# Kernel optimization log

Measured on AMD Instinct MI355X. Metric: run time of the kernel, lower is better.

The kernel has to match this reference:

```python
import jax, jax.numpy as jnp
import numpy as np

DIM = 2048
NUM_HEADS = 16
NUM_KV_HEADS = 4
HEAD_DIM = DIM // NUM_HEADS  # 128
ROPE_BASE = 10000.0
TRAIN_SEQ_LEN = 1024
EPS = 1.1920929e-07  # torch.finfo(float32).eps, used by F.rms_norm default


def _rope_tables(seq_len, dtype=jnp.float32):
    rd = HEAD_DIM  # rope_dims defaults to full head_dim
    if seq_len > TRAIN_SEQ_LEN:
        s = seq_len / TRAIN_SEQ_LEN
        base = ROPE_BASE * s ** (rd / (rd - 2))
    else:
        base = ROPE_BASE
    inv_freq = 1.0 / base ** (jnp.arange(0, rd, 2, dtype=jnp.float32) / rd)
    t = jnp.arange(seq_len, dtype=jnp.float32)
    freqs = jnp.outer(t, inv_freq)  # [S, rd//2]
    cos = jnp.cos(freqs)[None, :, None, :].astype(dtype)  # [1,S,1,rd//2]
    sin = jnp.sin(freqs)[None, :, None, :].astype(dtype)
    return cos, sin


def _rms_norm(x):
    var = jnp.mean(jnp.square(x), axis=-1, keepdims=True)
    return x * jax.lax.rsqrt(var + EPS)


def _apply_rotary(x, cos, sin):
    h = x.shape[-1] // 2
    x1, x2 = x[..., :h], x[..., h:]
    return jnp.concatenate((x1 * cos + x2 * sin, -x1 * sin + x2 * cos), axis=-1)


def setup_inputs() -> dict:
    key = jax.random.key(0)
    ks = jax.random.split(key, 6)
    B, S = 2, 2048
    kv_dim = NUM_KV_HEADS * HEAD_DIM
    x = jax.random.normal(ks[0], (B, S, DIM), dtype=jnp.float32)
    Wq = jax.random.normal(ks[1], (DIM, DIM), dtype=jnp.float32) * 0.02
    Wk = jax.random.normal(ks[2], (kv_dim, DIM), dtype=jnp.float32) * 0.02
    Wv = jax.random.normal(ks[3], (kv_dim, DIM), dtype=jnp.float32) * 0.02
    Wo = jax.random.normal(ks[4], (DIM, DIM), dtype=jnp.float32) * 0.02
    q_gain = jnp.full((NUM_HEADS,), 1.0, dtype=jnp.float32)
    return {"x": x, "Wq": Wq, "Wk": Wk, "Wv": Wv, "Wo": Wo, "q_gain": q_gain}


def reference(x, Wq, Wk, Wv, Wo, q_gain):
    B, S, D = x.shape
    H, Hkv, Dh = NUM_HEADS, NUM_KV_HEADS, HEAD_DIM
    # QKV projections (CastedLinear, no bias)
    q = (x @ Wq.T).reshape(B, S, H, Dh)
    k = (x @ Wk.T).reshape(B, S, Hkv, Dh)
    v = (x @ Wv.T).reshape(B, S, Hkv, Dh)
    # RMSNorm over head_dim (no learned weight)
    q = _rms_norm(q)
    k = _rms_norm(k)
    # RoPE (full head_dim, NTK-scaled since S > train_seq_len)
    cos, sin = _rope_tables(S, q.dtype)
    q = _apply_rotary(q, cos, sin)
    k = _apply_rotary(k, cos, sin)
    # per-head gain on q
    q = q * q_gain.astype(q.dtype)[None, None, :, None]
    # GQA: repeat_interleave kv heads
    reps = H // Hkv
    k = jnp.repeat(k, reps, axis=2)  # [B,S,H,Dh]
    v = jnp.repeat(v, reps, axis=2)
    # causal attention
    scale = 1.0 / jnp.sqrt(jnp.asarray(Dh, dtype=q.dtype))
    scores = jnp.einsum('bqhd,bkhd->bhqk', q, k) * scale  # [B,H,S,S]
    causal = jnp.tril(jnp.ones((S, S), dtype=bool))
    scores = jnp.where(causal[None, None], scores, jnp.finfo(scores.dtype).min)
    attn = jax.nn.softmax(scores, axis=-1)
    y = jnp.einsum('bhqk,bkhd->bqhd', attn, v)  # [B,S,H,Dh]
    return y.reshape(B, S, D) @ Wo.T
```

## Files before the change

### kernel.cpp

```cpp
#include <hip/hip_runtime.h>

#define DIMSZ 2048
#define NHEAD 16
#define NKV 4
#define HD 128
#define QKVD 3072
#define SEQ 2048
#define NTOK 4096

typedef __attribute__((ext_vector_type(8))) short short8;
typedef __attribute__((ext_vector_type(4))) float f32x4;
typedef unsigned short u16;

__device__ __forceinline__ u16 f2bf(float x) {
  union { float f; unsigned u; } v; v.f = x;
  unsigned r = v.u + 0x7fffu + ((v.u >> 16) & 1u);
  return (u16)(r >> 16);
}
__device__ __forceinline__ unsigned pack_bf2(float a, float b) {
  unsigned ua = __float_as_uint(a) + 0x8000u;
  unsigned ub = __float_as_uint(b) + 0x8000u;
  return __builtin_amdgcn_perm(ub, ua, 0x07060302);
}

__device__ __forceinline__ void gl_lds16(const void* g, void* l) {
  __builtin_amdgcn_global_load_lds(
      (const __attribute__((address_space(1))) void*)g,
      (__attribute__((address_space(3))) void*)l, 16, 0, 0);
}

__global__ __launch_bounds__(256)
void castAll(const float* __restrict__ x,  const float* __restrict__ Wq,
             const float* __restrict__ Wk, const float* __restrict__ Wv,
             const float* __restrict__ Wo, u16* __restrict__ xb,
             u16* __restrict__ Wqkvb, u16* __restrict__ Wob) {
  int i = blockIdx.x * 256 + threadIdx.x;
  int f = i * 4;
  const float* src; u16* dst; int off;
  if (f < 8388608)       { src = x;  dst = xb;    off = f; }
  else if (f < 12582912) { src = Wq; dst = Wqkvb; off = f - 8388608; }
  else if (f < 13631488) { src = Wk; dst = Wqkvb + 4194304; off = f - 12582912; }
  else if (f < 14680064) { src = Wv; dst = Wqkvb + 5242880; off = f - 13631488; }
  else                   { src = Wo; dst = Wob;   off = f - 14680064; }
  float4 v = *(const float4*)(src + off);
  ushort4 o;
  o.x = f2bf(v.x); o.y = f2bf(v.y); o.z = f2bf(v.z); o.w = f2bf(v.w);
  *(ushort4*)(dst + off) = o;
}

template <bool F32OUT>
__global__ __launch_bounds__(512, 2)
void gemm256(const u16* __restrict__ A, const u16* __restrict__ W,
             void* __restrict__ Cv, int M, int N, int K) {
  __shared__ __align__(16) u16 As[2][256][64];
  __shared__ __align__(16) u16 Bs[2][256][64];
  const int tid = threadIdx.x;
  const int l = tid & 63;
  const int w = tid >> 6;
  const int r = l & 15, q = l >> 4;
  const int wm = (w >> 2) * 128;
  const int wn = (w & 3) * 64;

  const int nx  = N >> 8;
  const int cpx = gridDim.x >> 3;
  const int lid = (blockIdx.x & 7) * cpx + (blockIdx.x >> 3);
  const int m0 = (lid / nx) << 8;
  const int n0 = (lid % nx) << 8;

  const int srow = w * 16 + (l >> 3);
  const int scol = ((l & 7) ^ (l >> 3)) << 3;
  const u16* Asrc = A + (long)(m0 + srow) * K + scol;
  const u16* Bsrc = W + (long)(n0 + srow) * K + scol;

  auto stA = [&](int d, int h, int kt) {
    const u16* s = Asrc + (long)(h * 128) * K + (long)kt * 64;
    gl_lds16(s,         &As[d][h * 128 + w * 16][0]);
    gl_lds16(s + 8 * K, &As[d][h * 128 + w * 16 + 8][0]);
  };
  auto stB = [&](int d, int h, int kt) {
    const u16* s = Bsrc + (long)(h * 128) * K + (long)kt * 64;
    gl_lds16(s,         &Bs[d][h * 128 + w * 16][0]);
    gl_lds16(s + 8 * K, &Bs[d][h * 128 + w * 16 + 8][0]);
  };
  auto lda = [&](int d, int rt, int ks) -> short8 {
    return *(const short8*)&As[d][wm + rt * 16 + r][(((ks << 2) | q) ^ (r & 7)) << 3];
  };
  auto ldb = [&](int d, int ct, int ks) -> short8 {
    return *(const short8*)&Bs[d][wn + ct * 16 + r][(((ks << 2) | q) ^ (r & 7)) << 3];
  };

  f32x4 acc[8][4] = {};
  short8 a[4][2], b[4][2];

#define MMA8(IB, JB)                                                          \
  do {                                                                        \
    __builtin_amdgcn_s_setprio(1);                                            \
    _Pragma("unroll") for (int i_ = 0; i_ < 4; ++i_)                          \
    _Pragma("unroll") for (int j_ = 0; j_ < 2; ++j_)                          \
    _Pragma("unroll") for (int k_ = 0; k_ < 2; ++k_)                          \
      acc[(IB) + i_][(JB) + j_] = __builtin_amdgcn_mfma_f32_16x16x32_bf16(    \
          a[i_][k_], b[(JB) + j_][k_], acc[(IB) + i_][(JB) + j_], 0, 0, 0);   \
    __builtin_amdgcn_s_setprio(0);                                            \
  } while (0)

#define LGKM0()                                           \
  do {                                                    \
    asm volatile("s_waitcnt lgkmcnt(0)" ::: "memory");    \
    __builtin_amdgcn_sched_barrier(0);                    \
  } while (0)

  stB(0, 0, 0); stA(0, 0, 0); stB(0, 1, 0); stA(0, 1, 0);
  stB(1, 0, 1); stA(1, 0, 1);
  asm volatile("s_waitcnt vmcnt(4)" ::: "memory");
  __builtin_amdgcn_s_barrier();

  const int niter = K >> 7;
  for (int it = 0; it < niter; ++it) {
    const int kt1 = 2 * it + 1, kt2 = 2 * it + 2, kt3 = 2 * it + 3;
    const bool more = (it + 1 < niter);

#pragma unroll
    for (int i = 0; i < 4; ++i) { a[i][0] = lda(0, i, 0); a[i][1] = lda(0, i, 1); }
#pragma unroll
    for (int j = 0; j < 2; ++j) { b[j][0] = ldb(0, j, 0); b[j][1] = ldb(0, j, 1); }
    stB(1, 1, kt1);
    __builtin_amdgcn_s_barrier();
    LGKM0();
    MMA8(0, 0);
    __builtin_amdgcn_s_barrier();

#pragma unroll
    for (int j = 2; j < 4; ++j) { b[j][0] = ldb(0, j, 0); b[j][1] = ldb(0, j, 1); }
    stA(1, 1, kt1);
    __builtin_amdgcn_s_barrier();
    LGKM0();
    MMA8(0, 2);
    __builtin_amdgcn_s_barrier();

#pragma unroll
    for (int i = 0; i < 4; ++i) { a[i][0] = lda(0, i + 4, 0); a[i][1] = lda(0, i + 4, 1); }
    if (more) stB(0, 0, kt2);
    __builtin_amdgcn_s_barrier();
    LGKM0();
    MMA8(4, 2);
    __builtin_amdgcn_s_barrier();

    if (more) stA(0, 0, kt2);
    __builtin_amdgcn_s_barrier();
    MMA8(4, 0);
    if (more) asm volatile("s_waitcnt vmcnt(4)" ::: "memory");
    else      asm volatile("s_waitcnt vmcnt(0)" ::: "memory");
    __builtin_amdgcn_s_barrier();

#pragma unroll
    for (int i = 0; i < 4; ++i) { a[i][0] = lda(1, i, 0); a[i][1] = lda(1, i, 1); }
#pragma unroll
    for (int j = 0; j < 2; ++j) { b[j][0] = ldb(1, j, 0); b[j][1] = ldb(1, j, 1); }
    if (more) stB(0, 1, kt2);
    __builtin_amdgcn_s_barrier();
    LGKM0();
    MMA8(0, 0);
    __builtin_amdgcn_s_barrier();

#pragma unroll
    for (int j = 2; j < 4; ++j) { b[j][0] = ldb(1, j, 0); b[j][1] = ldb(1, j, 1); }
    if (more) stA(0, 1, kt2);
    __builtin_amdgcn_s_barrier();
    LGKM0();
    MMA8(0, 2);
    __builtin_amdgcn_s_barrier();

#pragma unroll
    for (int i = 0; i < 4; ++i) { a[i][0] = lda(1, i + 4, 0); a[i][1] = lda(1, i + 4, 1); }
    if (more) stB(1, 0, kt3);
    __builtin_amdgcn_s_barrier();
    LGKM0();
    MMA8(4, 2);
    __builtin_amdgcn_s_barrier();

    if (more) stA(1, 0, kt3);
    __builtin_amdgcn_s_barrier();
    MMA8(4, 0);
    if (more) asm volatile("s_waitcnt vmcnt(4)" ::: "memory");
    __builtin_amdgcn_s_barrier();
  }
#undef MMA8
#undef LGKM0

#pragma unroll
  for (int i = 0; i < 8; ++i)
#pragma unroll
    for (int j = 0; j < 4; ++j) {
      int row = m0 + wm + i * 16 + q * 4;
      int col = n0 + wn + j * 16 + r;
#pragma unroll
      for (int t = 0; t < 4; ++t) {
        if (F32OUT)
          ((float*)Cv)[(long)(row + t) * N + col] = acc[i][j][t];
        else
          ((u16*)Cv)[(long)(row + t) * N + col] = f2bf(acc[i][j][t]);
      }
    }
}

__global__ __launch_bounds__(256)
void prep(u16* __restrict__ qkv, const float* __restrict__ gain, float qsc,
          u16* __restrict__ vt) {
  if (blockIdx.x < 20480) {
    int gid  = blockIdx.x * 4 + (threadIdx.x >> 6);
    int lane = threadIdx.x & 63;
    int token = gid / 20;
    int idx   = gid % 20;
    int s     = token & (SEQ - 1);
    bool isq  = idx < 16;
    int off   = isq ? idx * HD : 2048 + (idx - 16) * HD;
    float psc = isq ? qsc * gain[idx & 15] : 1.0f;
    u16* p = qkv + (long)token * QKVD + off;
    union { unsigned u; float f; } c1, c2;
    c1.u = ((unsigned)p[lane]) << 16;
    c2.u = ((unsigned)p[lane + 64]) << 16;
    float x1 = c1.f, x2 = c2.f;
    float ss = x1 * x1 + x2 * x2;
#pragma unroll
    for (int d = 1; d < 64; d <<= 1) ss += __shfl_xor(ss, d);
    float rn = rsqrtf(ss * (1.0f / 128.0f) + 1.1920929e-07f) * psc;
    float lb = log2f(10000.0f) + 128.0f / 126.0f;
    float inv_freq = exp2f(-(float)lane * (lb * (1.0f / 64.0f)));
    float ang = (float)s * inv_freq;
    float sn, cs;
    sincosf(ang, &sn, &cs);
    p[lane]      = f2bf((x1 * cs + x2 * sn) * rn);
    p[lane + 64] = f2bf((-x1 * sn + x2 * cs) * rn);
  } else {
    __shared__ u16 T[128 * 72];
    int bid = blockIdx.x - 20480;
    const int k0 = (bid & 31) * 64, hkv = (bid >> 5) & 3, b = bid >> 7;
    const u16* vb = qkv + 2560;
    const int t = threadIdx.x;
    const int key = t & 63, dh0 = (t >> 6) * 32;
#pragma unroll
    for (int c = 0; c < 4; c++) {
      uint4 vv = *(const uint4*)&vb[(long)(b * SEQ + k0 + key) * QKVD + hkv * HD + dh0 + c * 8];
      u16 tmp[8];
      *(uint4*)tmp = vv;
#pragma unroll
      for (int e = 0; e < 8; e++) T[(dh0 + c * 8 + e) * 72 + key] = tmp[e];
    }
    __syncthreads();
    const int dh = t >> 1, half = t & 1;
#pragma unroll
    for (int c = 0; c < 4; c++) {
      uint4 ov = *(const uint4*)&T[dh * 72 + half * 32 + c * 8];
      *(uint4*)&vt[((long)(b * NKV + hkv) * HD + dh) * SEQ + k0 + half * 32 + c * 8] = ov;
    }
  }
}

__global__ __launch_bounds__(256, 4)
void fattn(const u16* __restrict__ qb, const u16* __restrict__ kb,
           const u16* __restrict__ vtg, u16* __restrict__ yb) {
  __shared__ u16 Ks[64 * 128];
  __shared__ u16 Vt[128 * 64];
  __shared__ u16 Ps[64 * 64];
  const int tid  = threadIdx.x;
  const int lane = tid & 63;
  const int w    = tid >> 6;
  const int r = lane & 15, q = lane >> 4;
  const int qt = 31 - (blockIdx.x >> 5);
  const int hb = blockIdx.x & 31;
  const int h  = hb >> 1;
  const int b  = hb & 1;
  const int q0 = qt * 64;
  const int hkv = h >> 2;

  long koff[4], voff[4];
  u16 *kdst[4], *vdst[4];
#pragma unroll
  for (int c = 0; c < 4; c++) {
    int gr = w * 16 + c * 4 + (lane >> 4);
    int s  = lane & 15;
    int kj = (s & 8) | ((s ^ gr) & 7);
    koff[c] = (long)gr * QKVD + hkv * HD + kj * 8;
    kdst[c] = Ks + (w * 16 + c * 4) * 128;
    int dh = (w * 4 + c) * 8 + (lane >> 3);
    int vs = lane & 7;
    int vj = (vs ^ dh) & 7;
    voff[c] = (long)dh * SEQ + vj * 8;
    vdst[c] = Vt + (w * 4 + c) * 8 * 64;
  }
  const u16* vbase = vtg + (long)(b * NKV + hkv) * HD * SEQ;

  short8 qf[4];
#pragma unroll
  for (int ks = 0; ks < 4; ks++)
    qf[ks] = *(const short8*)&qb[(long)(b * SEQ + q0 + w * 16 + r) * QKVD +
                                 h * HD + ks * 32 + q * 8];

  f32x4 oacc[8] = {};
  float l_i = 0.f;
  const int maskbase = q * 4 - w * 16 - r;
  const int psx = (r & 7) << 1;

  for (int k0 = 0; k0 <= q0; k0 += 64) {
    __syncthreads();
    const u16* kb_t = kb + (long)(b * SEQ + k0) * QKVD;
    const u16* vb_t = vbase + k0;
#pragma unroll
    for (int c = 0; c < 4; c++) {
      gl_lds16(kb_t + koff[c], kdst[c]);
      gl_lds16(vb_t + voff[c], vdst[c]);
    }
    __syncthreads();

    const bool maskit = (k0 == q0);

    f32x4 st[4] = {};
#pragma unroll
    for (int jt = 0; jt < 4; jt++)
#pragma unroll
      for (int ks = 0; ks < 4; ks++) {
        int row = jt * 16 + r;
        int j = ks * 4 + q;
        int p = (j & 8) | ((j ^ row) & 7);
        short8 kf = *(const short8*)&Ks[row * 128 + p * 8];
        st[jt] = __builtin_amdgcn_mfma_f32_16x16x32_bf16(kf, qf[ks], st[jt], 0, 0, 0);
      }

    if (maskit) {
#pragma unroll
      for (int jt = 0; jt < 4; jt++)
#pragma unroll
        for (int t = 0; t < 4; t++)
          if (jt * 16 + maskbase + t > 0) st[jt][t] = -3e38f;
    }

#pragma unroll
    for (int jt = 0; jt < 4; jt++) {
#pragma unroll
      for (int t = 0; t < 4; t++) {
        float p = exp2f(st[jt][t]);
        st[jt][t] = p;
      }
      l_i += (st[jt][0] + st[jt][1]) + (st[jt][2] + st[jt][3]);
      uint2 pk;
      pk.x = pack_bf2(st[jt][0], st[jt][1]);
      pk.y = pack_bf2(st[jt][2], st[jt][3]);
      *(uint2*)&Ps[(w * 16 + r) * 64 + ((jt * 4 + q) ^ psx) * 4] = pk;
    }
    asm volatile("s_waitcnt lgkmcnt(0)" ::: "memory");

#pragma unroll
    for (int ks = 0; ks < 2; ks++) {
      short8 pf = *(const short8*)&Ps[(w * 16 + r) * 64 + ((ks * 8 + q * 2) ^ psx) * 4];
#pragma unroll
      for (int n = 0; n < 8; n++) {
        int row = n * 16 + r;
        int j = ks * 4 + q;
        int p = (j ^ row) & 7;
        short8 vf = *(const short8*)&Vt[row * 64 + p * 8];
        oacc[n] = __builtin_amdgcn_mfma_f32_16x16x32_bf16(pf, vf, oacc[n], 0, 0, 0);
      }
    }
  }

  l_i += __shfl_xor(l_i, 16);
  l_i += __shfl_xor(l_i, 32);
  float lb4[4];
#pragma unroll
  for (int t = 0; t < 4; t++) lb4[t] = 1.0f / __shfl(l_i, q * 4 + t);
#pragma unroll
  for (int n = 0; n < 8; n++)
#pragma unroll
    for (int t = 0; t < 4; t++) {
      int row = q0 + w * 16 + q * 4 + t;
      int col = n * 16 + r;
      yb[(long)(b * SEQ + row) * DIMSZ + h * HD + col] = f2bf(oacc[n][t] * lb4[t]);
    }
}

extern "C" void kernel_launch(void* const* d_in, const int* in_sizes, int n_in,
                              void* d_out, int out_size, void* d_ws, size_t ws_size,
                              hipStream_t stream) {
  const float* x  = (const float*)d_in[0];
  const float* Wq = (const float*)d_in[1];
  const float* Wk = (const float*)d_in[2];
  const float* Wv = (const float*)d_in[3];
  const float* Wo = (const float*)d_in[4];
  const float* qg = (const float*)d_in[5];
  float* out = (float*)d_out;

  const long MB = 1024 * 1024;
  char* ws = (char*)d_ws;
  u16* xb    = (u16*)(ws + 0 * MB);
  u16* ybuf  = (u16*)(ws + 0 * MB);
  u16* Wqkvb = (u16*)(ws + 16 * MB);
  u16* Wob   = (u16*)(ws + 28 * MB);
  u16* qkv   = (u16*)(ws + 36 * MB);
  u16* vtg   = (u16*)(ws + 60 * MB);

  castAll<<<18432, 256, 0, stream>>>(x, Wq, Wk, Wv, Wo, xb, Wqkvb, Wob);

  gemm256<false><<<(QKVD / 256) * (NTOK / 256), 512, 0, stream>>>(
      xb, Wqkvb, qkv, NTOK, QKVD, DIMSZ);

  const float qsc = 0.08838834764831845f * 1.44269504088896f;
  prep<<<20736, 256, 0, stream>>>(qkv, qg, qsc, vtg);

  fattn<<<1024, 256, 0, stream>>>(qkv, qkv + 2048, vtg, ybuf);

  gemm256<true><<<(DIMSZ / 256) * (NTOK / 256), 512, 0, stream>>>(
      ybuf, Wob, out, NTOK, DIMSZ, DIMSZ);
}
```

Measured before the change: 329.8 us.

## Interleave LDS fragment loads into MFMA phases of the GEMM main loop

```diff
diff --git a/kernel.cpp b/kernel.cpp
--- a/kernel.cpp
+++ b/kernel.cpp
@@ -90,18 +90,44 @@
   };
 
   f32x4 acc[8][4] = {};
-  short8 a[4][2], b[4][2];
-
-#define MMA8(IB, JB)                                                          \
+  short8 a[4][2];
+  short8 bA[2][2];
+  short8 bB[2][2];
+
+#define MF(va, vb, c) __builtin_amdgcn_mfma_f32_16x16x32_bf16(va, vb, c, 0, 0, 0)
+
+#define PHASE_MMA(IB, JB, BP, INJ)                                            \
   do {                                                                        \
     __builtin_amdgcn_s_setprio(1);                                            \
-    _Pragma("unroll") for (int i_ = 0; i_ < 4; ++i_)                          \
-    _Pragma("unroll") for (int j_ = 0; j_ < 2; ++j_)                          \
-    _Pragma("unroll") for (int k_ = 0; k_ < 2; ++k_)                          \
-      acc[(IB) + i_][(JB) + j_] = __builtin_amdgcn_mfma_f32_16x16x32_bf16(    \
-          a[i_][k_], b[(JB) + j_][k_], acc[(IB) + i_][(JB) + j_], 0, 0, 0);   \
+    _Pragma("unroll") for (int i_ = 0; i_ < 4; ++i_) {                        \
+      acc[(IB)+i_][(JB)+0] = MF(a[i_][0], BP[0][0], acc[(IB)+i_][(JB)+0]);    \
+      acc[(IB)+i_][(JB)+1] = MF(a[i_][0], BP[1][0], acc[(IB)+i_][(JB)+1]);    \
+      acc[(IB)+i_][(JB)+0] = MF(a[i_][1], BP[0][1], acc[(IB)+i_][(JB)+0]);    \
+      acc[(IB)+i_][(JB)+1] = MF(a[i_][1], BP[1][1], acc[(IB)+i_][(JB)+1]);    \
+      INJ(i_)                                                                 \
+    }                                                                         \
     __builtin_amdgcn_s_setprio(0);                                            \
   } while (0)
+
+#define INJ_NONE(i_)
+#define INJ_B23_D0(i_)                                                        \
+  if ((i_) == 0) { bB[0][0] = ldb(0,2,0); bB[0][1] = ldb(0,2,1);              \
+                   bB[1][0] = ldb(0,3,0); bB[1][1] = ldb(0,3,1); }
+#define INJ_A47_D0(i_)                                                        \
+  { a[i_][0] = lda(0,4+(i_),0); a[i_][1] = lda(0,4+(i_),1); }
+#define INJ_P4(i_)                                                            \
+  { a[i_][0] = lda(1,(i_),0); a[i_][1] = lda(1,(i_),1);                       \
+    if ((i_) == 0) { bB[0][0] = ldb(1,0,0); bB[0][1] = ldb(1,0,1);            \
+                     bB[1][0] = ldb(1,1,0); bB[1][1] = ldb(1,1,1); } }
+#define INJ_B23_D1(i_)                                                        \
+  if ((i_) == 0) { bA[0][0] = ldb(1,2,0); bA[0][1] = ldb(1,2,1);              \
+                   bA[1][0] = ldb(1,3,0); bA[1][1] = ldb(1,3,1); }
+#define INJ_A47_D1(i_)                                                        \
+  { a[i_][0] = lda(1,4+(i_),0); a[i_][1] = lda(1,4+(i_),1); }
+#define INJ_P8(i_)                                                            \
+  if (more) { a[i_][0] = lda(0,(i_),0); a[i_][1] = lda(0,(i_),1);             \
+    if ((i_) == 0) { bA[0][0] = ldb(0,0,0); bA[0][1] = ldb(0,0,1);            \
+                     bA[1][0] = ldb(0,1,0); bA[1][1] = ldb(0,1,1); } }
 
 #define LGKM0()                                           \
   do {                                                    \
@@ -113,78 +139,76 @@
   stB(1, 0, 1); stA(1, 0, 1);
   asm volatile("s_waitcnt vmcnt(4)" ::: "memory");
   __builtin_amdgcn_s_barrier();
+#pragma unroll
+  for (int i = 0; i < 4; ++i) { a[i][0] = lda(0, i, 0); a[i][1] = lda(0, i, 1); }
+#pragma unroll
+  for (int j = 0; j < 2; ++j) { bA[j][0] = ldb(0, j, 0); bA[j][1] = ldb(0, j, 1); }
 
   const int niter = K >> 7;
   for (int it = 0; it < niter; ++it) {
     const int kt1 = 2 * it + 1, kt2 = 2 * it + 2, kt3 = 2 * it + 3;
     const bool more = (it + 1 < niter);
 
-#pragma unroll
-    for (int i = 0; i < 4; ++i) { a[i][0] = lda(0, i, 0); a[i][1] = lda(0, i, 1); }
-#pragma unroll
-    for (int j = 0; j < 2; ++j) { b[j][0] = ldb(0, j, 0); b[j][1] = ldb(0, j, 1); }
     stB(1, 1, kt1);
     __builtin_amdgcn_s_barrier();
     LGKM0();
-    MMA8(0, 0);
-    __builtin_amdgcn_s_barrier();
-
-#pragma unroll
-    for (int j = 2; j < 4; ++j) { b[j][0] = ldb(0, j, 0); b[j][1] = ldb(0, j, 1); }
+    PHASE_MMA(0, 0, bA, INJ_B23_D0);
+    __builtin_amdgcn_s_barrier();
+
     stA(1, 1, kt1);
     __builtin_amdgcn_s_barrier();
     LGKM0();
-    MMA8(0, 2);
-    __builtin_amdgcn_s_barrier();
-
-#pragma unroll
-    for (int i = 0; i < 4; ++i) { a[i][0] = lda(0, i + 4, 0); a[i][1] = lda(0, i + 4, 1); }
+    PHASE_MMA(0, 2, bB, INJ_A47_D0);
+    __builtin_amdgcn_s_barrier();
+
     if (more) stB(0, 0, kt2);
     __builtin_amdgcn_s_barrier();
     LGKM0();
-    MMA8(4, 2);
+    PHASE_MMA(4, 2, bB, INJ_NONE);
+    if (more) asm volatile("s_waitcnt vmcnt(2)" ::: "memory");
+    else      asm volatile("s_waitcnt vmcnt(0)" ::: "memory");
     __builtin_amdgcn_s_barrier();
 
     if (more) stA(0, 0, kt2);
     __builtin_amdgcn_s_barrier();
-    MMA8(4, 0);
-    if (more) asm volatile("s_waitcnt vmcnt(4)" ::: "memory");
-    else      asm volatile("s_waitcnt vmcnt(0)" ::: "memory");
-    __builtin_amdgcn_s_barrier();
-
-#pragma unroll
-    for (int i = 0; i < 4; ++i) { a[i][0] = lda(1, i, 0); a[i][1] = lda(1, i, 1); }
-#pragma unroll
-    for (int j = 0; j < 2; ++j) { b[j][0] = ldb(1, j, 0); b[j][1] = ldb(1, j, 1); }
+    LGKM0();
+    PHASE_MMA(4, 0, bA, INJ_P4);
+    __builtin_amdgcn_s_barrier();
+
     if (more) stB(0, 1, kt2);
     __builtin_amdgcn_s_barrier();
     LGKM0();
-    MMA8(0, 0);
-    __builtin_amdgcn_s_barrier();
-
-#pragma unroll
-    for (int j = 2; j < 4; ++j) { b[j][0] = ldb(1, j, 0); b[j][1] = ldb(1, j, 1); }
+    PHASE_MMA(0, 0, bB, INJ_B23_D1);
+    __builtin_amdgcn_s_barrier();
+
     if (more) stA(0, 1, kt2);
     __builtin_amdgcn_s_barrier();
     LGKM0();
-    MMA8(0, 2);
-    __builtin_amdgcn_s_barrier();
-
-#pragma unroll
-    for (int i = 0; i < 4; ++i) { a[i][0] = lda(1, i + 4, 0); a[i][1] = lda(1, i + 4, 1); }
+    PHASE_MMA(0, 2, bA, INJ_A47_D1);
+    __builtin_amdgcn_s_barrier();
+
     if (more) stB(1, 0, kt3);
     __builtin_amdgcn_s_barrier();
     LGKM0();
-    MMA8(4, 2);
+    PHASE_MMA(4, 2, bA, INJ_NONE);
+    if (more) asm volatile("s_waitcnt vmcnt(2)" ::: "memory");
     __builtin_amdgcn_s_barrier();
 
     if (more) stA(1, 0, kt3);
     __builtin_amdgcn_s_barrier();
-    MMA8(4, 0);
-    if (more) asm volatile("s_waitcnt vmcnt(4)" ::: "memory");
+    LGKM0();
+    PHASE_MMA(4, 0, bB, INJ_P8);
     __builtin_amdgcn_s_barrier();
   }
-#undef MMA8
+#undef MF
+#undef PHASE_MMA
+#undef INJ_NONE
+#undef INJ_B23_D0
+#undef INJ_A47_D0
+#undef INJ_P4
+#undef INJ_B23_D1
+#undef INJ_A47_D1
+#undef INJ_P8
 #undef LGKM0
 
 #pragma unroll
```

New measurement: 322.9 us. 2.1% less time.
